# Kernel optimization log

Hardware: AMD Instinct MI355X
Metric: run time of the kernel (lower is better)

## Reference

```python
import jax, jax.numpy as jnp
import numpy as np

NEG_SLOPE = 0.2  # PyG GATv2Conv default leaky_relu negative slope


def _gatv2_layer(x, src, dst, n, Wl, bl, Wr, br, att, bias, concat):
    # PyG GATv2Conv (share_weights=False, edge_dim=None):
    #   x_l = lin_l(x) on source, x_r = lin_r(x) on target
    #   m = leaky_relu(x_l[src] + x_r[dst]); alpha = softmax_dst(<m, att>)
    #   out[i] = sum_{e: dst=i} alpha_e * x_l[src_e]
    H, C = att.shape
    xl = (x @ Wl + bl).reshape(n, H, C)
    xr = (x @ Wr + br).reshape(n, H, C)
    m = jax.nn.leaky_relu(xl[src] + xr[dst], NEG_SLOPE)      # [E,H,C]
    logits = jnp.einsum('ehc,hc->eh', m, att)                # [E,H]
    lmax = jax.ops.segment_max(logits, dst, num_segments=n)  # [N,H]
    e = jnp.exp(logits - lmax[dst])
    denom = jax.ops.segment_sum(e, dst, num_segments=n)
    alpha = e / (denom[dst] + 1e-16)                         # [E,H]
    out = jax.ops.segment_sum(xl[src] * alpha[:, :, None], dst, num_segments=n)
    out = out.reshape(n, H * C) if concat else out.mean(axis=1)
    return out + bias


def _glorot(key, shape):
    fan_in, fan_out = shape[0], shape[-1]
    s = jnp.sqrt(6.0 / (fan_in + fan_out))
    return jax.random.uniform(key, shape, jnp.float32, -s, s)


def setup_inputs() -> dict:
    key = jax.random.key(0)
    N, E, B = 50000, 800000, 512
    node_in, hidden, heads, meta_dim = 128, 32, 4, 12
    ks = jax.random.split(key, 32)
    inp = {
        'x': jax.random.normal(ks[0], (N, node_in), jnp.float32),
        'edge_index': jax.random.randint(ks[1], (2, E), 0, N, jnp.int64),
        'batch': jnp.sort(jax.random.randint(ks[2], (N,), 0, B, jnp.int64)),
        'metadata': jax.random.normal(ks[3], (B, meta_dim), jnp.float32),
    }
    dims = [(node_in, hidden, heads), (hidden * heads, hidden, heads), (hidden * heads, hidden, 1)]
    i = 4
    for li, (din, dh, H) in enumerate(dims):
        inp[f'Wl{li}'] = _glorot(ks[i], (din, H * dh)); i += 1
        inp[f'bl{li}'] = jnp.zeros((H * dh,), jnp.float32)
        inp[f'Wr{li}'] = _glorot(ks[i], (din, H * dh)); i += 1
        inp[f'br{li}'] = jnp.zeros((H * dh,), jnp.float32)
        inp[f'att{li}'] = _glorot(ks[i], (H, dh)); i += 1
        out_dim = H * dh if li < 2 else dh  # last layer concat=False
        inp[f'b{li}'] = jnp.zeros((out_dim,), jnp.float32)
    pool_dim = hidden  # n_layers=3 -> final single-head layer
    inp['Wh1'] = _glorot(ks[i], (pool_dim + meta_dim, pool_dim)); i += 1
    inp['bh1'] = jnp.zeros((pool_dim,), jnp.float32)
    inp['Wh2'] = _glorot(ks[i], (pool_dim, 1)); i += 1
    inp['bh2'] = jnp.zeros((1,), jnp.float32)
    return inp


def reference(x, edge_index, batch, metadata,
              Wl0, bl0, Wr0, br0, att0, b0,
              Wl1, bl1, Wr1, br1, att1, b1,
              Wl2, bl2, Wr2, br2, att2, b2,
              Wh1, bh1, Wh2, bh2):
    n = x.shape[0]
    B = metadata.shape[0]
    # PyG GATv2Conv add_self_loops=True
    loop = jnp.arange(n, dtype=edge_index.dtype)
    src = jnp.concatenate([edge_index[0], loop])
    dst = jnp.concatenate([edge_index[1], loop])
    params = [(Wl0, bl0, Wr0, br0, att0, b0, True),
              (Wl1, bl1, Wr1, br1, att1, b1, True),
              (Wl2, bl2, Wr2, br2, att2, b2, False)]
    h = x
    for (Wl, bl, Wr, br, att, bias, concat) in params:
        h = _gatv2_layer(h, src, dst, n, Wl, bl, Wr, br, att, bias, concat)
        h = jax.nn.elu(h)  # dropout is identity in eval mode
    # global mean pool over graphs
    sums = jax.ops.segment_sum(h, batch, num_segments=B)
    cnt = jax.ops.segment_sum(jnp.ones((n,), h.dtype), batch, num_segments=B)
    emb = sums / jnp.clip(cnt, 1.0)[:, None]
    z = jnp.concatenate([emb, metadata], axis=1)
    z = jax.nn.relu(z @ Wh1 + bh1)
    return z @ Wh2 + bh2  # (B, 1) logits
```

## Files before the change

kernel.cpp:

```cpp
#include <hip/hip_runtime.h>
#include <cstdint>
#include <cstddef>

#define NEG_SLOPE 0.2f
#define LOG2E 1.44269504f
#define NBLK 256

typedef __attribute__((ext_vector_type(8))) short short8;
typedef __attribute__((ext_vector_type(4))) float f32x4;

__device__ __forceinline__ float bf2f(unsigned short u) {
    union { unsigned int i; float f; } x; x.i = ((unsigned int)u) << 16; return x.f;
}
__device__ __forceinline__ unsigned short f2bf(float f) {
    union { float f; unsigned int i; } x;
    x.f = f;
    unsigned int u = x.i;
    return (unsigned short)((u + 0x7FFFu + ((u >> 16) & 1u)) >> 16);
}

__device__ __forceinline__ float dpp_sum8(float p) {
    p += __int_as_float(__builtin_amdgcn_update_dpp(0, __float_as_int(p), 0xB1, 0xF, 0xF, true));
    p += __int_as_float(__builtin_amdgcn_update_dpp(0, __float_as_int(p), 0x4E, 0xF, 0xF, true));
    p += __int_as_float(__builtin_amdgcn_update_dpp(0, __float_as_int(p), 0x141, 0xF, 0xF, true));
    return p;
}

__global__ __launch_bounds__(256) void prep_w_all(
    const float* __restrict__ Wl0, const float* __restrict__ Wr0,
    const float* __restrict__ Wl1, const float* __restrict__ Wr1,
    const float* __restrict__ Wl2, const float* __restrict__ Wr2,
    unsigned short* __restrict__ Bt0, unsigned short* __restrict__ Bt1,
    unsigned short* __restrict__ Bt2)
{
    int idx = blockIdx.x * 256 + threadIdx.x;
    const int SZ = 256 * 128;
    const float *Wl, *Wr; unsigned short* Bt; int dout;
    if (idx < SZ)              { Wl = Wl0; Wr = Wr0; Bt = Bt0; dout = 128; }
    else if (idx < 2 * SZ)     { Wl = Wl1; Wr = Wr1; Bt = Bt1; dout = 128; idx -= SZ; }
    else if (idx < 2 * SZ + 64 * 128) { Wl = Wl2; Wr = Wr2; Bt = Bt2; dout = 32; idx -= 2 * SZ; }
    else return;
    int n = idx >> 7, k = idx & 127;
    float v = (n < dout) ? Wl[(size_t)k * dout + n] : Wr[(size_t)k * dout + (n - dout)];
    Bt[idx] = f2bf(v);
}

template<int BN, bool ABF16>
__global__ __launch_bounds__(256) void gemm_mfma(
    const void* __restrict__ Avoid, int M,
    const unsigned short* __restrict__ Bt,
    const float* __restrict__ bl, const float* __restrict__ br,
    int dout, unsigned short* __restrict__ XL, unsigned short* __restrict__ XR)
{
    constexpr int LDA = 136;
    constexpr int NT  = BN / 16;
    __shared__ __attribute__((aligned(16))) unsigned short Bs[BN * LDA];
    const int t  = threadIdx.x;
    const int m0 = blockIdx.x * 64;
    const int n0 = blockIdx.y * BN;

    const int w    = t >> 6;
    const int lane = t & 63;
    const int fr   = lane & 15;
    const int quad = lane >> 4;

#pragma unroll
    for (int i = 0; i < BN / 16; ++i) {
        int c  = t + i * 256;
        int n  = c >> 4;
        int kc = (c & 15) * 8;
        *(short8*)(Bs + n * LDA + kc) =
            *(const short8*)(Bt + (size_t)(n0 + n) * 128 + kc);
    }

    const int arow = m0 + w * 16 + fr;
    const size_t abase = (size_t)(arow < M ? arow : 0) * 128 + quad * 8;
    short8 afr[4];
    if (ABF16) {
        const unsigned short* A = (const unsigned short*)Avoid;
#pragma unroll
        for (int kk = 0; kk < 4; ++kk)
            afr[kk] = *(const short8*)(A + abase + kk * 32);
    } else {
        const float* A = (const float*)Avoid;
#pragma unroll
        for (int kk = 0; kk < 4; ++kk) {
            float4 lo = *(const float4*)(A + abase + kk * 32);
            float4 hi = *(const float4*)(A + abase + kk * 32 + 4);
            afr[kk][0] = (short)f2bf(lo.x); afr[kk][1] = (short)f2bf(lo.y);
            afr[kk][2] = (short)f2bf(lo.z); afr[kk][3] = (short)f2bf(lo.w);
            afr[kk][4] = (short)f2bf(hi.x); afr[kk][5] = (short)f2bf(hi.y);
            afr[kk][6] = (short)f2bf(hi.z); afr[kk][7] = (short)f2bf(hi.w);
        }
    }
    __syncthreads();

    f32x4 acc[NT] = {};
    const unsigned short* bp = Bs + fr * LDA + quad * 8;
#pragma unroll
    for (int kk = 0; kk < 4; ++kk) {
#pragma unroll
        for (int j = 0; j < NT; ++j) {
            short8 bfr = *(const short8*)(bp + j * 16 * LDA + kk * 32);
            acc[j] = __builtin_amdgcn_mfma_f32_16x16x32_bf16(afr[kk], bfr, acc[j], 0, 0, 0);
        }
    }

#pragma unroll
    for (int j = 0; j < NT; ++j) {
        int col = n0 + j * 16 + fr;
        float bias = (col < dout) ? bl[col] : br[col - dout];
#pragma unroll
        for (int r = 0; r < 4; ++r) {
            int row = m0 + w * 16 + quad * 4 + r;
            if (row < M) {
                unsigned short o = f2bf(acc[j][r] + bias);
                if (col < dout) XL[(size_t)row * dout + col] = o;
                else            XR[(size_t)row * dout + (col - dout)] = o;
            }
        }
    }
}

__global__ __launch_bounds__(256) void csr_hist(
    const int* __restrict__ dst, int E, int tile, int* __restrict__ hist)
{
    __shared__ int h[256];
    const int t = threadIdx.x, b = blockIdx.x;
    h[t] = 0;
    __syncthreads();
    const int e0 = b * tile;
    const int e1 = min(E, e0 + tile);
    for (int e = e0 + t; e < e1; e += 256)
        atomicAdd(&h[dst[e] >> 8], 1);
    __syncthreads();
    hist[t * NBLK + b] = h[t];
}

__global__ __launch_bounds__(256) void csr_scatter(
    const int* __restrict__ src, const int* __restrict__ dst, int E, int tile,
    const int* __restrict__ hist_s, unsigned int* __restrict__ sorted)
{
    __shared__ int cur[256];
    const int t = threadIdx.x, b = blockIdx.x;
    cur[t] = hist_s[t * NBLK + b];
    __syncthreads();
    const int e0 = b * tile;
    const int e1 = min(E, e0 + tile);
    for (int e = e0 + t; e < e1; e += 256) {
        int d = dst[e];
        int pos = atomicAdd(&cur[d >> 8], 1);
        sorted[pos] = ((unsigned int)d << 16) | (unsigned int)src[e];
    }
}

__global__ __launch_bounds__(256) void csr_fine(
    const unsigned int* __restrict__ sorted, int E, int N,
    const int* __restrict__ hist_s,
    int* __restrict__ rowptr, unsigned short* __restrict__ csr_src)
{
    __shared__ int h[256];
    __shared__ int sc[256];
    const int t = threadIdx.x, d = blockIdx.x;
    const int start = hist_s[d * NBLK];
    const int end   = (d < 255) ? hist_s[(d + 1) * NBLK] : E;
    h[t] = 0;
    __syncthreads();
    for (int e = start + t; e < end; e += 256)
        atomicAdd(&h[(sorted[e] >> 16) & 0xFF], 1);
    __syncthreads();
    int v = h[t];
    sc[t] = v;
    __syncthreads();
    for (int off = 1; off < 256; off <<= 1) {
        int u = (t >= off) ? sc[t - off] : 0;
        __syncthreads();
        sc[t] += u;
        __syncthreads();
    }
    const int base = start + sc[t] - v;
    const int node = (d << 8) + t;
    if (node <= N) rowptr[node] = base;
    h[t] = base;
    __syncthreads();
    for (int e = start + t; e < end; e += 256) {
        unsigned int it = sorted[e];
        int pos = atomicAdd(&h[(it >> 16) & 0xFF], 1);
        csr_src[pos] = (unsigned short)(it & 0xFFFFu);
    }
}

__global__ __launch_bounds__(256) void scan_partial(
    const int* __restrict__ cnt, int N, int* __restrict__ bsum)
{
    __shared__ int red[4];
    const int t = threadIdx.x;
    const int base = blockIdx.x * 2048;
    int s = 0;
#pragma unroll
    for (int i = 0; i < 8; ++i) {
        int idx = base + t + i * 256;
        if (idx < N) s += cnt[idx];
    }
#pragma unroll
    for (int off = 32; off >= 1; off >>= 1) s += __shfl_xor(s, off);
    if ((t & 63) == 0) red[t >> 6] = s;
    __syncthreads();
    if (t == 0) bsum[blockIdx.x] = red[0] + red[1] + red[2] + red[3];
}

__global__ __launch_bounds__(256) void scan_bsums(
    int* __restrict__ bsum, int nb, int E, int* __restrict__ rowptr, int N)
{
    __shared__ int sh[256];
    const int t = threadIdx.x;
    int v = (t < nb) ? bsum[t] : 0;
    sh[t] = v;
    __syncthreads();
    for (int off = 1; off < 256; off <<= 1) {
        int u = (t >= off) ? sh[t - off] : 0;
        __syncthreads();
        sh[t] += u;
        __syncthreads();
    }
    if (t < nb) bsum[t] = sh[t] - v;
    if (t == 0) rowptr[N] = E;
}

__global__ __launch_bounds__(256) void scan_final(
    const int* __restrict__ cnt, int N, const int* __restrict__ bsum,
    int* __restrict__ rowptr)
{
    __shared__ int sdat[2048];
    __shared__ int tsum[256];
    const int t = threadIdx.x;
    const int base = blockIdx.x * 2048;
#pragma unroll
    for (int i = 0; i < 8; ++i) {
        int idx = base + t + i * 256;
        sdat[t + i * 256] = (idx < N) ? cnt[idx] : 0;
    }
    __syncthreads();
    int vals[8];
    int s = 0;
#pragma unroll
    for (int j = 0; j < 8; ++j) { vals[j] = sdat[t * 8 + j]; s += vals[j]; }
    tsum[t] = s;
    __syncthreads();
    for (int off = 1; off < 256; off <<= 1) {
        int u = (t >= off) ? tsum[t - off] : 0;
        __syncthreads();
        tsum[t] += u;
        __syncthreads();
    }
    int run = bsum[blockIdx.x] + tsum[t] - s;
#pragma unroll
    for (int j = 0; j < 8; ++j) { sdat[t * 8 + j] = run; run += vals[j]; }
    __syncthreads();
#pragma unroll
    for (int i = 0; i < 8; ++i) {
        int idx = base + t + i * 256;
        if (idx < N) rowptr[idx] = sdat[t + i * 256];
    }
}

template<int H>
__global__ __launch_bounds__(256, 4) void gat_fused(
    const unsigned short* __restrict__ xl, const unsigned short* __restrict__ xr,
    const int* __restrict__ rowptr, const unsigned short* __restrict__ csr_src,
    const float* __restrict__ att, const float* __restrict__ bias,
    unsigned short* __restrict__ hout, int hstride, int N)
{
    constexpr int HC  = 32 * H;
    constexpr int LPE = HC / 4;
    constexpr int EPW = 64 / LPE;
    const int node = blockIdx.x * 4 + (threadIdx.x >> 6);
    if (node >= N) return;
    const int lane = threadIdx.x & 63;
    const int q    = lane % LPE;
    const int slot = lane / LPE;
    const int rs   = rowptr[node];
    const int re   = rowptr[node + 1];

    const unsigned short* __restrict__ xlb = xl + 4 * q;
    float4 xri;
    {
        ushort4 u = *(const ushort4*)(xr + (size_t)node * HC + 4 * q);
        xri.x = bf2f(u.x); xri.y = bf2f(u.y); xri.z = bf2f(u.z); xri.w = bf2f(u.w);
    }
    float4 b1, b2;
    {
        float4 a = *(const float4*)(att + 4 * q);
        const float c1 = 0.5f * (1.0f + NEG_SLOPE) * LOG2E;
        const float c2 = 0.5f * (1.0f - NEG_SLOPE) * LOG2E;
        b1.x = a.x * c1; b1.y = a.y * c1; b1.z = a.z * c1; b1.w = a.w * c1;
        b2.x = a.x * c2; b2.y = a.y * c2; b2.z = a.z * c2; b2.w = a.w * c2;
    }

    float l = 0.f;
    float4 acc = make_float4(0.f, 0.f, 0.f, 0.f);

    auto ld4 = [&](int s) -> float4 {
        ushort4 u = *(const ushort4*)(xlb + (size_t)s * HC);
        float4 v;
        v.x = bf2f(u.x); v.y = bf2f(u.y); v.z = bf2f(u.z); v.w = bf2f(u.w);
        return v;
    };

    auto edge_w = [&](const float4& v) -> float {
        float sx = v.x + xri.x, sy = v.y + xri.y, sz = v.z + xri.z, sw = v.w + xri.w;
        float p  = b1.x * sx;
        float pq = b2.x * fabsf(sx);
        p  = fmaf(b1.y, sy, p);
        pq = fmaf(b2.y, fabsf(sy), pq);
        p  = fmaf(b1.z, sz, p);
        pq = fmaf(b2.z, fabsf(sz), pq);
        p  = fmaf(b1.w, sw, p);
        pq = fmaf(b2.w, fabsf(sw), pq);
        p += pq;
        p = dpp_sum8(p);
        return exp2f(p);
    };

    if (slot == 0) {
        float4 v = ld4(node);
        float w = edge_w(v);
        l = w;
        acc.x = w * v.x; acc.y = w * v.y; acc.z = w * v.z; acc.w = w * v.w;
    }

    int k = rs + slot;
    for (; k + EPW < re; k += 2 * EPW) {
        int s0 = csr_src[k];
        int s1 = csr_src[k + EPW];
        float4 v0 = ld4(s0);
        float4 v1 = ld4(s1);
        float w0 = edge_w(v0);
        float w1 = edge_w(v1);
        l += w0 + w1;
        acc.x = fmaf(w0, v0.x, fmaf(w1, v1.x, acc.x));
        acc.y = fmaf(w0, v0.y, fmaf(w1, v1.y, acc.y));
        acc.z = fmaf(w0, v0.z, fmaf(w1, v1.z, acc.z));
        acc.w = fmaf(w0, v0.w, fmaf(w1, v1.w, acc.w));
    }
    if (k < re) {
        int s0 = csr_src[k];
        float4 v0 = ld4(s0);
        float w0 = edge_w(v0);
        l += w0;
        acc.x = fmaf(w0, v0.x, acc.x);
        acc.y = fmaf(w0, v0.y, acc.y);
        acc.z = fmaf(w0, v0.z, acc.z);
        acc.w = fmaf(w0, v0.w, acc.w);
    }

#pragma unroll
    for (int mask = LPE; mask < 64; mask <<= 1) {
        l     += __shfl_xor(l, mask);
        acc.x += __shfl_xor(acc.x, mask);
        acc.y += __shfl_xor(acc.y, mask);
        acc.z += __shfl_xor(acc.z, mask);
        acc.w += __shfl_xor(acc.w, mask);
    }

    if (lane < LPE) {
        const float4 bi = *(const float4*)(bias + 4 * q);
        float inv = 1.f / (l + 1e-16f);
        float4 o;
        o.x = acc.x * inv + bi.x;
        o.y = acc.y * inv + bi.y;
        o.z = acc.z * inv + bi.z;
        o.w = acc.w * inv + bi.w;
        o.x = (o.x > 0.f) ? o.x : expm1f(o.x);
        o.y = (o.y > 0.f) ? o.y : expm1f(o.y);
        o.z = (o.z > 0.f) ? o.z : expm1f(o.z);
        o.w = (o.w > 0.f) ? o.w : expm1f(o.w);
        ushort4 ob;
        ob.x = f2bf(o.x); ob.y = f2bf(o.y); ob.z = f2bf(o.z); ob.w = f2bf(o.w);
        *(ushort4*)(hout + (size_t)node * hstride + 4 * q) = ob;
    }
}

__global__ __launch_bounds__(128) void pool_head_kernel(
    const unsigned short* __restrict__ h, int hstride,
    const int* __restrict__ batch, int N,
    const float* __restrict__ meta,
    const float* __restrict__ Wh1, const float* __restrict__ bh1,
    const float* __restrict__ Wh2, const float* __restrict__ bh2,
    float* __restrict__ out)
{
    const int b = blockIdx.x;
    const int t = threadIdx.x;
    __shared__ float s[128];
    __shared__ float z[44];

    int lo = 0, hi = N;
    while (lo < hi) { int mid = (lo + hi) >> 1; if (batch[mid] < b) lo = mid + 1; else hi = mid; }
    int lo2 = lo, hi2 = N;
    while (lo2 < hi2) { int mid = (lo2 + hi2) >> 1; if (batch[mid] < b + 1) lo2 = mid + 1; else hi2 = mid; }
    const int start = lo, end = lo2;

    const int c = t & 31, r = t >> 5;
    float acc = 0.f;
    for (int row = start + r; row < end; row += 4)
        acc += bf2f(h[(size_t)row * hstride + c]);
    s[t] = acc;
    __syncthreads();
    if (t < 32) {
        float sum = s[t] + s[t + 32] + s[t + 64] + s[t + 96];
        z[t] = sum / fmaxf((float)(end - start), 1.0f);
    } else if (t < 44) {
        z[t] = meta[(size_t)b * 12 + (t - 32)];
    }
    __syncthreads();
    if (t < 32) {
        float hj = bh1[t];
#pragma unroll
        for (int k = 0; k < 44; ++k)
            hj = fmaf(z[k], Wh1[k * 32 + t], hj);
        hj = fmaxf(hj, 0.f);
        float p = hj * Wh2[t];
#pragma unroll
        for (int off = 16; off >= 1; off >>= 1)
            p += __shfl_xor(p, off, 32);
        if (t == 0) out[b] = p + bh2[0];
    }
}

extern "C" void kernel_launch(void* const* d_in, const int* in_sizes, int n_in,
                              void* d_out, int out_size, void* d_ws, size_t ws_size,
                              hipStream_t stream)
{
    const float* x     = (const float*)d_in[0];
    const int*   ei    = (const int*)d_in[1];
    const int*   batch = (const int*)d_in[2];
    const float* meta  = (const float*)d_in[3];
    const float* Wl[3]  = {(const float*)d_in[4],  (const float*)d_in[10], (const float*)d_in[16]};
    const float* bl[3]  = {(const float*)d_in[5],  (const float*)d_in[11], (const float*)d_in[17]};
    const float* Wr[3]  = {(const float*)d_in[6],  (const float*)d_in[12], (const float*)d_in[18]};
    const float* br[3]  = {(const float*)d_in[7],  (const float*)d_in[13], (const float*)d_in[19]};
    const float* att[3] = {(const float*)d_in[8],  (const float*)d_in[14], (const float*)d_in[20]};
    const float* bb[3]  = {(const float*)d_in[9],  (const float*)d_in[15], (const float*)d_in[21]};
    const float* Wh1 = (const float*)d_in[22];
    const float* bh1 = (const float*)d_in[23];
    const float* Wh2 = (const float*)d_in[24];
    const float* bh2 = (const float*)d_in[25];
    float* out = (float*)d_out;

    const int N  = in_sizes[0] / 128;
    const int E  = in_sizes[1] / 2;
    const int B  = in_sizes[3] / 12;

    char* wsp = (char*)d_ws;
    size_t off_ = 0;
    auto alloc = [&](size_t bytes) {
        char* p = wsp + off_;
        off_ = (off_ + bytes + 255) & ~(size_t)255;
        return p;
    };
    unsigned short* xlbuf = (unsigned short*)alloc((size_t)N * 128 * 2);
    unsigned short* xrbuf = (unsigned short*)alloc((size_t)N * 128 * 2);
    unsigned short* hbuf  = (unsigned short*)alloc((size_t)N * 128 * 2);
    int*   rowptr  = (int*)alloc((size_t)(N + 1) * 4);
    unsigned short* csr_src = (unsigned short*)alloc((size_t)E * 2);
    unsigned int*   sorted  = (unsigned int*)alloc((size_t)E * 4);
    int*   hist_g  = (int*)alloc((size_t)65536 * 4);
    int*   hist_s  = (int*)alloc((size_t)65537 * 4);
    unsigned short* Bt0     = (unsigned short*)alloc((size_t)256 * 128 * 2);
    unsigned short* Bt1     = (unsigned short*)alloc((size_t)256 * 128 * 2);
    unsigned short* Bt2     = (unsigned short*)alloc((size_t)64 * 128 * 2);
    int*   bsum    = (int*)alloc((size_t)256 * 4);

    const int* srcI = ei;
    const int* dstI = ei + E;

    prep_w_all<<<(2 * 256 * 128 + 64 * 128 + 255) / 256, 256, 0, stream>>>(
        Wl[0], Wr[0], Wl[1], Wr[1], Wl[2], Wr[2], Bt0, Bt1, Bt2);

    const int tile = (E + NBLK - 1) / NBLK;
    csr_hist<<<NBLK, 256, 0, stream>>>(dstI, E, tile, hist_g);
    scan_partial<<<32, 256, 0, stream>>>(hist_g, 65536, bsum);
    scan_bsums<<<1, 256, 0, stream>>>(bsum, 32, E, hist_s, 65536);
    scan_final<<<32, 256, 0, stream>>>(hist_g, 65536, bsum, hist_s);
    csr_scatter<<<NBLK, 256, 0, stream>>>(srcI, dstI, E, tile, hist_s, sorted);
    csr_fine<<<(N >> 8) + 1, 256, 0, stream>>>(sorted, E, N, hist_s, rowptr, csr_src);

    const int GB = (N + 3) / 4;
    const int MB = (N + 63) / 64;

    {
        gemm_mfma<128, false><<<dim3(MB, 2), 256, 0, stream>>>(x, N, Bt0, bl[0], br[0], 128, xlbuf, xrbuf);
        gat_fused<4><<<GB, 256, 0, stream>>>(xlbuf, xrbuf, rowptr, csr_src, att[0], bb[0], hbuf, 128, N);
    }
    {
        gemm_mfma<128, true><<<dim3(MB, 2), 256, 0, stream>>>(hbuf, N, Bt1, bl[1], br[1], 128, xlbuf, xrbuf);
        gat_fused<4><<<GB, 256, 0, stream>>>(xlbuf, xrbuf, rowptr, csr_src, att[1], bb[1], hbuf, 128, N);
    }
    {
        gemm_mfma<64, true><<<dim3(MB, 1), 256, 0, stream>>>(hbuf, N, Bt2, bl[2], br[2], 32, xlbuf, xrbuf);
        gat_fused<1><<<GB, 256, 0, stream>>>(xlbuf, xrbuf, rowptr, csr_src, att[2], bb[2], hbuf, 32, N);
    }
    pool_head_kernel<<<B, 128, 0, stream>>>(hbuf, 32, batch, N, meta, Wh1, bh1, Wh2, bh2, out);
}
```

Baseline: 340.8 us.

## Merge all stages into one cooperative persistent megakernel with grid syncs

Result: slower. 1.147 ms (+236.5%).

```diff
diff --git a/kernel.cpp b/kernel.cpp
--- a/kernel.cpp
+++ b/kernel.cpp
@@ -1,10 +1,13 @@
 #include <hip/hip_runtime.h>
+#include <hip/hip_cooperative_groups.h>
 #include <cstdint>
 #include <cstddef>
 
+namespace cg = cooperative_groups;
+
 #define NEG_SLOPE 0.2f
 #define LOG2E 1.44269504f
-#define NBLK 256
+#define SMEM_BYTES 17408
 
 typedef __attribute__((ext_vector_type(8))) short short8;
 typedef __attribute__((ext_vector_type(4))) float f32x4;
@@ -26,223 +29,56 @@
     return p;
 }
 
-__global__ __launch_bounds__(256) void prep_w_all(
-    const float* __restrict__ Wl0, const float* __restrict__ Wr0,
-    const float* __restrict__ Wl1, const float* __restrict__ Wr1,
-    const float* __restrict__ Wl2, const float* __restrict__ Wr2,
-    unsigned short* __restrict__ Bt0, unsigned short* __restrict__ Bt1,
-    unsigned short* __restrict__ Bt2)
-{
-    int idx = blockIdx.x * 256 + threadIdx.x;
+struct KParams {
+    const float* x; const int* srcI; const int* dstI; const int* batch; const float* meta;
+    const float *Wl0, *bl0, *Wr0, *br0, *att0, *b0;
+    const float *Wl1, *bl1, *Wr1, *br1, *att1, *b1;
+    const float *Wl2, *bl2, *Wr2, *br2, *att2, *b2;
+    const float *Wh1, *bh1, *Wh2, *bh2;
+    float* out;
+    unsigned short *xlbuf, *xrbuf, *hbuf, *csr_src, *Bt0, *Bt1, *Bt2;
+    int *rowptr, *hist_g, *hist_s, *bsum;
+    unsigned int* sorted;
+    int N, E, B, tile;
+};
+
+
+__device__ __forceinline__ void phase_prep_hist(const KParams& p, unsigned char* smem) {
+    const int t = threadIdx.x;
+    int* h = (int*)smem;
+    if (blockIdx.x < 256) {
+        h[t] = 0;
+        __syncthreads();
+        const int e0 = blockIdx.x * p.tile;
+        const int e1 = min(p.E, e0 + p.tile);
+        for (int e = e0 + t; e < e1; e += 256)
+            atomicAdd(&h[p.dstI[e] >> 8], 1);
+        __syncthreads();
+        p.hist_g[t * 256 + blockIdx.x] = h[t];
+    }
     const int SZ = 256 * 128;
-    const float *Wl, *Wr; unsigned short* Bt; int dout;
-    if (idx < SZ)              { Wl = Wl0; Wr = Wr0; Bt = Bt0; dout = 128; }
-    else if (idx < 2 * SZ)     { Wl = Wl1; Wr = Wr1; Bt = Bt1; dout = 128; idx -= SZ; }
-    else if (idx < 2 * SZ + 64 * 128) { Wl = Wl2; Wr = Wr2; Bt = Bt2; dout = 32; idx -= 2 * SZ; }
-    else return;
-    int n = idx >> 7, k = idx & 127;
-    float v = (n < dout) ? Wl[(size_t)k * dout + n] : Wr[(size_t)k * dout + (n - dout)];
-    Bt[idx] = f2bf(v);
-}
-
-template<int BN, bool ABF16>
-__global__ __launch_bounds__(256) void gemm_mfma(
-    const void* __restrict__ Avoid, int M,
-    const unsigned short* __restrict__ Bt,
-    const float* __restrict__ bl, const float* __restrict__ br,
-    int dout, unsigned short* __restrict__ XL, unsigned short* __restrict__ XR)
-{
-    constexpr int LDA = 136;
-    constexpr int NT  = BN / 16;
-    __shared__ __attribute__((aligned(16))) unsigned short Bs[BN * LDA];
-    const int t  = threadIdx.x;
-    const int m0 = blockIdx.x * 64;
-    const int n0 = blockIdx.y * BN;
-
-    const int w    = t >> 6;
-    const int lane = t & 63;
-    const int fr   = lane & 15;
-    const int quad = lane >> 4;
-
-#pragma unroll
-    for (int i = 0; i < BN / 16; ++i) {
-        int c  = t + i * 256;
-        int n  = c >> 4;
-        int kc = (c & 15) * 8;
-        *(short8*)(Bs + n * LDA + kc) =
-            *(const short8*)(Bt + (size_t)(n0 + n) * 128 + kc);
-    }
-
-    const int arow = m0 + w * 16 + fr;
-    const size_t abase = (size_t)(arow < M ? arow : 0) * 128 + quad * 8;
-    short8 afr[4];
-    if (ABF16) {
-        const unsigned short* A = (const unsigned short*)Avoid;
-#pragma unroll
-        for (int kk = 0; kk < 4; ++kk)
-            afr[kk] = *(const short8*)(A + abase + kk * 32);
-    } else {
-        const float* A = (const float*)Avoid;
-#pragma unroll
-        for (int kk = 0; kk < 4; ++kk) {
-            float4 lo = *(const float4*)(A + abase + kk * 32);
-            float4 hi = *(const float4*)(A + abase + kk * 32 + 4);
-            afr[kk][0] = (short)f2bf(lo.x); afr[kk][1] = (short)f2bf(lo.y);
-            afr[kk][2] = (short)f2bf(lo.z); afr[kk][3] = (short)f2bf(lo.w);
-            afr[kk][4] = (short)f2bf(hi.x); afr[kk][5] = (short)f2bf(hi.y);
-            afr[kk][6] = (short)f2bf(hi.z); afr[kk][7] = (short)f2bf(hi.w);
-        }
-    }
-    __syncthreads();
-
-    f32x4 acc[NT] = {};
-    const unsigned short* bp = Bs + fr * LDA + quad * 8;
-#pragma unroll
-    for (int kk = 0; kk < 4; ++kk) {
-#pragma unroll
-        for (int j = 0; j < NT; ++j) {
-            short8 bfr = *(const short8*)(bp + j * 16 * LDA + kk * 32);
-            acc[j] = __builtin_amdgcn_mfma_f32_16x16x32_bf16(afr[kk], bfr, acc[j], 0, 0, 0);
-        }
-    }
-
-#pragma unroll
-    for (int j = 0; j < NT; ++j) {
-        int col = n0 + j * 16 + fr;
-        float bias = (col < dout) ? bl[col] : br[col - dout];
-#pragma unroll
-        for (int r = 0; r < 4; ++r) {
-            int row = m0 + w * 16 + quad * 4 + r;
-            if (row < M) {
-                unsigned short o = f2bf(acc[j][r] + bias);
-                if (col < dout) XL[(size_t)row * dout + col] = o;
-                else            XR[(size_t)row * dout + (col - dout)] = o;
-            }
-        }
-    }
-}
-
-__global__ __launch_bounds__(256) void csr_hist(
-    const int* __restrict__ dst, int E, int tile, int* __restrict__ hist)
-{
-    __shared__ int h[256];
-    const int t = threadIdx.x, b = blockIdx.x;
-    h[t] = 0;
-    __syncthreads();
-    const int e0 = b * tile;
-    const int e1 = min(E, e0 + tile);
-    for (int e = e0 + t; e < e1; e += 256)
-        atomicAdd(&h[dst[e] >> 8], 1);
-    __syncthreads();
-    hist[t * NBLK + b] = h[t];
-}
-
-__global__ __launch_bounds__(256) void csr_scatter(
-    const int* __restrict__ src, const int* __restrict__ dst, int E, int tile,
-    const int* __restrict__ hist_s, unsigned int* __restrict__ sorted)
-{
-    __shared__ int cur[256];
-    const int t = threadIdx.x, b = blockIdx.x;
-    cur[t] = hist_s[t * NBLK + b];
-    __syncthreads();
-    const int e0 = b * tile;
-    const int e1 = min(E, e0 + tile);
-    for (int e = e0 + t; e < e1; e += 256) {
-        int d = dst[e];
-        int pos = atomicAdd(&cur[d >> 8], 1);
-        sorted[pos] = ((unsigned int)d << 16) | (unsigned int)src[e];
-    }
-}
-
-__global__ __launch_bounds__(256) void csr_fine(
-    const unsigned int* __restrict__ sorted, int E, int N,
-    const int* __restrict__ hist_s,
-    int* __restrict__ rowptr, unsigned short* __restrict__ csr_src)
-{
-    __shared__ int h[256];
-    __shared__ int sc[256];
-    const int t = threadIdx.x, d = blockIdx.x;
-    const int start = hist_s[d * NBLK];
-    const int end   = (d < 255) ? hist_s[(d + 1) * NBLK] : E;
-    h[t] = 0;
-    __syncthreads();
-    for (int e = start + t; e < end; e += 256)
-        atomicAdd(&h[(sorted[e] >> 16) & 0xFF], 1);
-    __syncthreads();
-    int v = h[t];
-    sc[t] = v;
-    __syncthreads();
-    for (int off = 1; off < 256; off <<= 1) {
-        int u = (t >= off) ? sc[t - off] : 0;
-        __syncthreads();
-        sc[t] += u;
-        __syncthreads();
-    }
-    const int base = start + sc[t] - v;
-    const int node = (d << 8) + t;
-    if (node <= N) rowptr[node] = base;
-    h[t] = base;
-    __syncthreads();
-    for (int e = start + t; e < end; e += 256) {
-        unsigned int it = sorted[e];
-        int pos = atomicAdd(&h[(it >> 16) & 0xFF], 1);
-        csr_src[pos] = (unsigned short)(it & 0xFFFFu);
-    }
-}
-
-__global__ __launch_bounds__(256) void scan_partial(
-    const int* __restrict__ cnt, int N, int* __restrict__ bsum)
-{
-    __shared__ int red[4];
+    for (int idx0 = blockIdx.x * 256 + t; idx0 < 2 * SZ + 64 * 128; idx0 += gridDim.x * 256) {
+        int idx = idx0;
+        const float *Wl, *Wr; unsigned short* Bt; int dout;
+        if (idx < SZ)          { Wl = p.Wl0; Wr = p.Wr0; Bt = p.Bt0; dout = 128; }
+        else if (idx < 2 * SZ) { Wl = p.Wl1; Wr = p.Wr1; Bt = p.Bt1; dout = 128; idx -= SZ; }
+        else                   { Wl = p.Wl2; Wr = p.Wr2; Bt = p.Bt2; dout = 32;  idx -= 2 * SZ; }
+        int n = idx >> 7, k = idx & 127;
+        float v = (n < dout) ? Wl[(size_t)k * dout + n] : Wr[(size_t)k * dout + (n - dout)];
+        Bt[idx] = f2bf(v);
+    }
+}
+
+__device__ __forceinline__ void phase_scanA(const KParams& p, unsigned char* smem) {
+    if (blockIdx.x >= 32) return;
+    int* sdat = (int*)smem;
+    int* tsum = (int*)(smem + 8192);
     const int t = threadIdx.x;
     const int base = blockIdx.x * 2048;
-    int s = 0;
-#pragma unroll
-    for (int i = 0; i < 8; ++i) {
-        int idx = base + t + i * 256;
-        if (idx < N) s += cnt[idx];
-    }
-#pragma unroll
-    for (int off = 32; off >= 1; off >>= 1) s += __shfl_xor(s, off);
-    if ((t & 63) == 0) red[t >> 6] = s;
+#pragma unroll
+    for (int i = 0; i < 8; ++i) sdat[t + i * 256] = p.hist_g[base + t + i * 256];
     __syncthreads();
-    if (t == 0) bsum[blockIdx.x] = red[0] + red[1] + red[2] + red[3];
-}
-
-__global__ __launch_bounds__(256) void scan_bsums(
-    int* __restrict__ bsum, int nb, int E, int* __restrict__ rowptr, int N)
-{
-    __shared__ int sh[256];
-    const int t = threadIdx.x;
-    int v = (t < nb) ? bsum[t] : 0;
-    sh[t] = v;
-    __syncthreads();
-    for (int off = 1; off < 256; off <<= 1) {
-        int u = (t >= off) ? sh[t - off] : 0;
-        __syncthreads();
-        sh[t] += u;
-        __syncthreads();
-    }
-    if (t < nb) bsum[t] = sh[t] - v;
-    if (t == 0) rowptr[N] = E;
-}
-
-__global__ __launch_bounds__(256) void scan_final(
-    const int* __restrict__ cnt, int N, const int* __restrict__ bsum,
-    int* __restrict__ rowptr)
-{
-    __shared__ int sdat[2048];
-    __shared__ int tsum[256];
-    const int t = threadIdx.x;
-    const int base = blockIdx.x * 2048;
-#pragma unroll
-    for (int i = 0; i < 8; ++i) {
-        int idx = base + t + i * 256;
-        sdat[t + i * 256] = (idx < N) ? cnt[idx] : 0;
-    }
-    __syncthreads();
-    int vals[8];
-    int s = 0;
+    int vals[8]; int s = 0;
 #pragma unroll
     for (int j = 0; j < 8; ++j) { vals[j] = sdat[t * 8 + j]; s += vals[j]; }
     tsum[t] = s;
@@ -253,19 +89,169 @@
         tsum[t] += u;
         __syncthreads();
     }
-    int run = bsum[blockIdx.x] + tsum[t] - s;
+    if (t == 0) p.bsum[blockIdx.x] = tsum[255];
+    int run = tsum[t] - s;
 #pragma unroll
     for (int j = 0; j < 8; ++j) { sdat[t * 8 + j] = run; run += vals[j]; }
     __syncthreads();
 #pragma unroll
-    for (int i = 0; i < 8; ++i) {
-        int idx = base + t + i * 256;
-        if (idx < N) rowptr[idx] = sdat[t + i * 256];
+    for (int i = 0; i < 8; ++i) p.hist_s[base + t + i * 256] = sdat[t + i * 256];
+}
+
+__device__ __forceinline__ void phase_scanB(const KParams& p) {
+    const int t = threadIdx.x;
+    if (blockIdx.x == 0 && t < 32) {
+        int o = p.bsum[t];
+        int v = o;
+#pragma unroll
+        for (int off = 1; off < 32; off <<= 1) {
+            int u = __shfl_up(v, off);
+            if (t >= off) v += u;
+        }
+        p.bsum[t] = v - o;
+    }
+}
+
+__device__ __forceinline__ void phase_scanC(const KParams& p) {
+    if (blockIdx.x >= 32) return;
+    const int t = threadIdx.x;
+    const int add = p.bsum[blockIdx.x];
+    const int base = blockIdx.x * 2048;
+#pragma unroll
+    for (int i = 0; i < 8; ++i) p.hist_s[base + t + i * 256] += add;
+}
+
+__device__ __forceinline__ void phase_scatter(const KParams& p, unsigned char* smem) {
+    if (blockIdx.x >= 256) return;
+    int* cur = (int*)smem;
+    const int t = threadIdx.x;
+    cur[t] = p.hist_s[t * 256 + blockIdx.x];
+    __syncthreads();
+    const int e0 = blockIdx.x * p.tile;
+    const int e1 = min(p.E, e0 + p.tile);
+    for (int e = e0 + t; e < e1; e += 256) {
+        int d = p.dstI[e];
+        int pos = atomicAdd(&cur[d >> 8], 1);
+        p.sorted[pos] = ((unsigned int)d << 16) | (unsigned int)p.srcI[e];
+    }
+}
+
+__device__ __forceinline__ void phase_fine(const KParams& p, unsigned char* smem) {
+    int* h  = (int*)smem;
+    int* sc = (int*)(smem + 1024);
+    const int t = threadIdx.x;
+    const int nb = (p.N >> 8) + 1;
+    for (int d = blockIdx.x; d < nb; d += gridDim.x) {
+        __syncthreads();
+        const int start = p.hist_s[d * 256];
+        const int end   = (d < 255) ? p.hist_s[(d + 1) * 256] : p.E;
+        h[t] = 0;
+        __syncthreads();
+        for (int e = start + t; e < end; e += 256)
+            atomicAdd(&h[(p.sorted[e] >> 16) & 0xFF], 1);
+        __syncthreads();
+        int v = h[t];
+        sc[t] = v;
+        __syncthreads();
+        for (int off = 1; off < 256; off <<= 1) {
+            int u = (t >= off) ? sc[t - off] : 0;
+            __syncthreads();
+            sc[t] += u;
+            __syncthreads();
+        }
+        const int base = start + sc[t] - v;
+        const int node = (d << 8) + t;
+        if (node <= p.N) p.rowptr[node] = base;
+        h[t] = base;
+        __syncthreads();
+        for (int e = start + t; e < end; e += 256) {
+            unsigned int it = p.sorted[e];
+            int pos = atomicAdd(&h[(it >> 16) & 0xFF], 1);
+            p.csr_src[pos] = (unsigned short)(it & 0xFFFFu);
+        }
+    }
+}
+
+__device__ __forceinline__ void gemm_phase(
+    const void* Avoid, int M, bool abf16,
+    const unsigned short* __restrict__ Bt,
+    const float* __restrict__ bl, const float* __restrict__ br,
+    int dout, int lognyt, unsigned short* __restrict__ XL, unsigned short* __restrict__ XR,
+    unsigned char* smem)
+{
+    unsigned short* Bs = (unsigned short*)smem;
+    const int t    = threadIdx.x;
+    const int w    = t >> 6;
+    const int lane = t & 63;
+    const int fr   = lane & 15;
+    const int quad = lane >> 4;
+    const int mb = (M + 63) >> 6;
+    const int ntiles = mb << lognyt;
+    const int nymask = (1 << lognyt) - 1;
+
+    for (int tid = blockIdx.x; tid < ntiles; tid += gridDim.x) {
+        const int m0 = (tid >> lognyt) * 64;
+        const int n0 = (tid & nymask) * 64;
+        __syncthreads();
+#pragma unroll
+        for (int i = 0; i < 4; ++i) {
+            int c  = t + i * 256;
+            int n  = c >> 4;
+            int kc = (c & 15) * 8;
+            *(short8*)(Bs + n * 136 + kc) =
+                *(const short8*)(Bt + (size_t)(n0 + n) * 128 + kc);
+        }
+        const int arow = m0 + w * 16 + fr;
+        const size_t abase = (size_t)(arow < M ? arow : 0) * 128 + quad * 8;
+        short8 afr[4];
+        if (abf16) {
+            const unsigned short* A = (const unsigned short*)Avoid;
+#pragma unroll
+            for (int kk = 0; kk < 4; ++kk)
+                afr[kk] = *(const short8*)(A + abase + kk * 32);
+        } else {
+            const float* A = (const float*)Avoid;
+#pragma unroll
+            for (int kk = 0; kk < 4; ++kk) {
+                float4 lo = *(const float4*)(A + abase + kk * 32);
+                float4 hi = *(const float4*)(A + abase + kk * 32 + 4);
+                afr[kk][0] = (short)f2bf(lo.x); afr[kk][1] = (short)f2bf(lo.y);
+                afr[kk][2] = (short)f2bf(lo.z); afr[kk][3] = (short)f2bf(lo.w);
+                afr[kk][4] = (short)f2bf(hi.x); afr[kk][5] = (short)f2bf(hi.y);
+                afr[kk][6] = (short)f2bf(hi.z); afr[kk][7] = (short)f2bf(hi.w);
+            }
+        }
+        __syncthreads();
+
+        f32x4 acc[4] = {};
+        const unsigned short* bp = Bs + fr * 136 + quad * 8;
+#pragma unroll
+        for (int kk = 0; kk < 4; ++kk) {
+#pragma unroll
+            for (int j = 0; j < 4; ++j) {
+                short8 bfr = *(const short8*)(bp + j * 16 * 136 + kk * 32);
+                acc[j] = __builtin_amdgcn_mfma_f32_16x16x32_bf16(afr[kk], bfr, acc[j], 0, 0, 0);
+            }
+        }
+#pragma unroll
+        for (int j = 0; j < 4; ++j) {
+            int col = n0 + j * 16 + fr;
+            float bias = (col < dout) ? bl[col] : br[col - dout];
+#pragma unroll
+            for (int r = 0; r < 4; ++r) {
+                int row = m0 + w * 16 + quad * 4 + r;
+                if (row < M) {
+                    unsigned short o = f2bf(acc[j][r] + bias);
+                    if (col < dout) XL[(size_t)row * dout + col] = o;
+                    else            XR[(size_t)row * dout + (col - dout)] = o;
+                }
+            }
+        }
     }
 }
 
 template<int H>
-__global__ __launch_bounds__(256, 4) void gat_fused(
+__device__ __forceinline__ void gat_phase(
     const unsigned short* __restrict__ xl, const unsigned short* __restrict__ xr,
     const int* __restrict__ rowptr, const unsigned short* __restrict__ csr_src,
     const float* __restrict__ att, const float* __restrict__ bias,
@@ -274,179 +260,218 @@
     constexpr int HC  = 32 * H;
     constexpr int LPE = HC / 4;
     constexpr int EPW = 64 / LPE;
-    const int node = blockIdx.x * 4 + (threadIdx.x >> 6);
-    if (node >= N) return;
-    const int lane = threadIdx.x & 63;
-    const int q    = lane % LPE;
-    const int slot = lane / LPE;
-    const int rs   = rowptr[node];
-    const int re   = rowptr[node + 1];
-
-    const unsigned short* __restrict__ xlb = xl + 4 * q;
-    float4 xri;
-    {
-        ushort4 u = *(const ushort4*)(xr + (size_t)node * HC + 4 * q);
-        xri.x = bf2f(u.x); xri.y = bf2f(u.y); xri.z = bf2f(u.z); xri.w = bf2f(u.w);
-    }
-    float4 b1, b2;
-    {
-        float4 a = *(const float4*)(att + 4 * q);
-        const float c1 = 0.5f * (1.0f + NEG_SLOPE) * LOG2E;
-        const float c2 = 0.5f * (1.0f - NEG_SLOPE) * LOG2E;
-        b1.x = a.x * c1; b1.y = a.y * c1; b1.z = a.z * c1; b1.w = a.w * c1;
-        b2.x = a.x * c2; b2.y = a.y * c2; b2.z = a.z * c2; b2.w = a.w * c2;
-    }
-
-    float l = 0.f;
-    float4 acc = make_float4(0.f, 0.f, 0.f, 0.f);
-
-    auto ld4 = [&](int s) -> float4 {
-        ushort4 u = *(const ushort4*)(xlb + (size_t)s * HC);
-        float4 v;
-        v.x = bf2f(u.x); v.y = bf2f(u.y); v.z = bf2f(u.z); v.w = bf2f(u.w);
-        return v;
-    };
-
-    auto edge_w = [&](const float4& v) -> float {
-        float sx = v.x + xri.x, sy = v.y + xri.y, sz = v.z + xri.z, sw = v.w + xri.w;
-        float p  = b1.x * sx;
-        float pq = b2.x * fabsf(sx);
-        p  = fmaf(b1.y, sy, p);
-        pq = fmaf(b2.y, fabsf(sy), pq);
-        p  = fmaf(b1.z, sz, p);
-        pq = fmaf(b2.z, fabsf(sz), pq);
-        p  = fmaf(b1.w, sw, p);
-        pq = fmaf(b2.w, fabsf(sw), pq);
-        p += pq;
-        p = dpp_sum8(p);
-        return exp2f(p);
-    };
-
-    if (slot == 0) {
-        float4 v = ld4(node);
-        float w = edge_w(v);
-        l = w;
-        acc.x = w * v.x; acc.y = w * v.y; acc.z = w * v.z; acc.w = w * v.w;
-    }
-
-    int k = rs + slot;
-    for (; k + EPW < re; k += 2 * EPW) {
-        int s0 = csr_src[k];
-        int s1 = csr_src[k + EPW];
-        float4 v0 = ld4(s0);
-        float4 v1 = ld4(s1);
-        float w0 = edge_w(v0);
-        float w1 = edge_w(v1);
-        l += w0 + w1;
-        acc.x = fmaf(w0, v0.x, fmaf(w1, v1.x, acc.x));
-        acc.y = fmaf(w0, v0.y, fmaf(w1, v1.y, acc.y));
-        acc.z = fmaf(w0, v0.z, fmaf(w1, v1.z, acc.z));
-        acc.w = fmaf(w0, v0.w, fmaf(w1, v1.w, acc.w));
-    }
-    if (k < re) {
-        int s0 = csr_src[k];
-        float4 v0 = ld4(s0);
-        float w0 = edge_w(v0);
-        l += w0;
-        acc.x = fmaf(w0, v0.x, acc.x);
-        acc.y = fmaf(w0, v0.y, acc.y);
-        acc.z = fmaf(w0, v0.z, acc.z);
-        acc.w = fmaf(w0, v0.w, acc.w);
-    }
-
-#pragma unroll
-    for (int mask = LPE; mask < 64; mask <<= 1) {
-        l     += __shfl_xor(l, mask);
-        acc.x += __shfl_xor(acc.x, mask);
-        acc.y += __shfl_xor(acc.y, mask);
-        acc.z += __shfl_xor(acc.z, mask);
-        acc.w += __shfl_xor(acc.w, mask);
-    }
-
-    if (lane < LPE) {
-        const float4 bi = *(const float4*)(bias + 4 * q);
-        float inv = 1.f / (l + 1e-16f);
-        float4 o;
-        o.x = acc.x * inv + bi.x;
-        o.y = acc.y * inv + bi.y;
-        o.z = acc.z * inv + bi.z;
-        o.w = acc.w * inv + bi.w;
-        o.x = (o.x > 0.f) ? o.x : expm1f(o.x);
-        o.y = (o.y > 0.f) ? o.y : expm1f(o.y);
-        o.z = (o.z > 0.f) ? o.z : expm1f(o.z);
-        o.w = (o.w > 0.f) ? o.w : expm1f(o.w);
-        ushort4 ob;
-        ob.x = f2bf(o.x); ob.y = f2bf(o.y); ob.z = f2bf(o.z); ob.w = f2bf(o.w);
-        *(ushort4*)(hout + (size_t)node * hstride + 4 * q) = ob;
-    }
-}
-
-__global__ __launch_bounds__(128) void pool_head_kernel(
-    const unsigned short* __restrict__ h, int hstride,
-    const int* __restrict__ batch, int N,
-    const float* __restrict__ meta,
-    const float* __restrict__ Wh1, const float* __restrict__ bh1,
-    const float* __restrict__ Wh2, const float* __restrict__ bh2,
-    float* __restrict__ out)
-{
-    const int b = blockIdx.x;
-    const int t = threadIdx.x;
-    __shared__ float s[128];
-    __shared__ float z[44];
-
-    int lo = 0, hi = N;
-    while (lo < hi) { int mid = (lo + hi) >> 1; if (batch[mid] < b) lo = mid + 1; else hi = mid; }
-    int lo2 = lo, hi2 = N;
-    while (lo2 < hi2) { int mid = (lo2 + hi2) >> 1; if (batch[mid] < b + 1) lo2 = mid + 1; else hi2 = mid; }
-    const int start = lo, end = lo2;
-
-    const int c = t & 31, r = t >> 5;
-    float acc = 0.f;
-    for (int row = start + r; row < end; row += 4)
-        acc += bf2f(h[(size_t)row * hstride + c]);
-    s[t] = acc;
-    __syncthreads();
-    if (t < 32) {
-        float sum = s[t] + s[t + 32] + s[t + 64] + s[t + 96];
-        z[t] = sum / fmaxf((float)(end - start), 1.0f);
-    } else if (t < 44) {
-        z[t] = meta[(size_t)b * 12 + (t - 32)];
-    }
-    __syncthreads();
-    if (t < 32) {
-        float hj = bh1[t];
-#pragma unroll
-        for (int k = 0; k < 44; ++k)
-            hj = fmaf(z[k], Wh1[k * 32 + t], hj);
-        hj = fmaxf(hj, 0.f);
-        float p = hj * Wh2[t];
-#pragma unroll
-        for (int off = 16; off >= 1; off >>= 1)
-            p += __shfl_xor(p, off, 32);
-        if (t == 0) out[b] = p + bh2[0];
-    }
+    const int ngrp = (N + 3) >> 2;
+    for (int grp = blockIdx.x; grp < ngrp; grp += gridDim.x) {
+        const int node = grp * 4 + (threadIdx.x >> 6);
+        if (node >= N) continue;
+        const int lane = threadIdx.x & 63;
+        const int q    = lane % LPE;
+        const int slot = lane / LPE;
+        const int rs   = rowptr[node];
+        const int re   = rowptr[node + 1];
+
+        const unsigned short* __restrict__ xlb = xl + 4 * q;
+        float4 xri;
+        {
+            ushort4 u = *(const ushort4*)(xr + (size_t)node * HC + 4 * q);
+            xri.x = bf2f(u.x); xri.y = bf2f(u.y); xri.z = bf2f(u.z); xri.w = bf2f(u.w);
+        }
+        float4 b1, b2;
+        {
+            float4 a = *(const float4*)(att + 4 * q);
+            const float c1 = 0.5f * (1.0f + NEG_SLOPE) * LOG2E;
+            const float c2 = 0.5f * (1.0f - NEG_SLOPE) * LOG2E;
+            b1.x = a.x * c1; b1.y = a.y * c1; b1.z = a.z * c1; b1.w = a.w * c1;
+            b2.x = a.x * c2; b2.y = a.y * c2; b2.z = a.z * c2; b2.w = a.w * c2;
+        }
+
+        float l = 0.f;
+        float4 acc = make_float4(0.f, 0.f, 0.f, 0.f);
+
+        auto ld4 = [&](int s) -> float4 {
+            ushort4 u = *(const ushort4*)(xlb + (size_t)s * HC);
+            float4 v;
+            v.x = bf2f(u.x); v.y = bf2f(u.y); v.z = bf2f(u.z); v.w = bf2f(u.w);
+            return v;
+        };
+        auto edge_w = [&](const float4& v) -> float {
+            float sx = v.x + xri.x, sy = v.y + xri.y, sz = v.z + xri.z, sw = v.w + xri.w;
+            float p  = b1.x * sx;
+            float pq = b2.x * fabsf(sx);
+            p  = fmaf(b1.y, sy, p);
+            pq = fmaf(b2.y, fabsf(sy), pq);
+            p  = fmaf(b1.z, sz, p);
+            pq = fmaf(b2.z, fabsf(sz), pq);
+            p  = fmaf(b1.w, sw, p);
+            pq = fmaf(b2.w, fabsf(sw), pq);
+            p += pq;
+            p = dpp_sum8(p);
+            return exp2f(p);
+        };
+
+        if (slot == 0) {
+            float4 v = ld4(node);
+            float w = edge_w(v);
+            l = w;
+            acc.x = w * v.x; acc.y = w * v.y; acc.z = w * v.z; acc.w = w * v.w;
+        }
+        int k = rs + slot;
+        for (; k + EPW < re; k += 2 * EPW) {
+            int s0 = csr_src[k];
+            int s1 = csr_src[k + EPW];
+            float4 v0 = ld4(s0);
+            float4 v1 = ld4(s1);
+            float w0 = edge_w(v0);
+            float w1 = edge_w(v1);
+            l += w0 + w1;
+            acc.x = fmaf(w0, v0.x, fmaf(w1, v1.x, acc.x));
+            acc.y = fmaf(w0, v0.y, fmaf(w1, v1.y, acc.y));
+            acc.z = fmaf(w0, v0.z, fmaf(w1, v1.z, acc.z));
+            acc.w = fmaf(w0, v0.w, fmaf(w1, v1.w, acc.w));
+        }
+        if (k < re) {
+            int s0 = csr_src[k];
+            float4 v0 = ld4(s0);
+            float w0 = edge_w(v0);
+            l += w0;
+            acc.x = fmaf(w0, v0.x, acc.x);
+            acc.y = fmaf(w0, v0.y, acc.y);
+            acc.z = fmaf(w0, v0.z, acc.z);
+            acc.w = fmaf(w0, v0.w, acc.w);
+        }
+#pragma unroll
+        for (int mask = LPE; mask < 64; mask <<= 1) {
+            l     += __shfl_xor(l, mask);
+            acc.x += __shfl_xor(acc.x, mask);
+            acc.y += __shfl_xor(acc.y, mask);
+            acc.z += __shfl_xor(acc.z, mask);
+            acc.w += __shfl_xor(acc.w, mask);
+        }
+        if (lane < LPE) {
+            const float4 bi = *(const float4*)(bias + 4 * q);
+            float inv = 1.f / (l + 1e-16f);
+            float4 o;
+            o.x = acc.x * inv + bi.x;
+            o.y = acc.y * inv + bi.y;
+            o.z = acc.z * inv + bi.z;
+            o.w = acc.w * inv + bi.w;
+            o.x = (o.x > 0.f) ? o.x : expm1f(o.x);
+            o.y = (o.y > 0.f) ? o.y : expm1f(o.y);
+            o.z = (o.z > 0.f) ? o.z : expm1f(o.z);
+            o.w = (o.w > 0.f) ? o.w : expm1f(o.w);
+            ushort4 ob;
+            ob.x = f2bf(o.x); ob.y = f2bf(o.y); ob.z = f2bf(o.z); ob.w = f2bf(o.w);
+            *(ushort4*)(hout + (size_t)node * hstride + 4 * q) = ob;
+        }
+    }
+}
+
+__device__ __forceinline__ void pool_phase(const KParams& p, unsigned char* smem) {
+    float* s = (float*)smem;
+    float* z = (float*)(smem + 1024);
+    const int t    = threadIdx.x;
+    const int half = t >> 7;
+    const int tl   = t & 127;
+    for (int g0 = blockIdx.x * 2; g0 < p.B; g0 += gridDim.x * 2) {
+        __syncthreads();
+        const int b = g0 + half;
+        const bool active = b < p.B;
+        int start = 0, end = 0;
+        if (active) {
+            int lo = 0, hi = p.N;
+            while (lo < hi) { int mid = (lo + hi) >> 1; if (p.batch[mid] < b) lo = mid + 1; else hi = mid; }
+            int lo2 = lo, hi2 = p.N;
+            while (lo2 < hi2) { int mid = (lo2 + hi2) >> 1; if (p.batch[mid] < b + 1) lo2 = mid + 1; else hi2 = mid; }
+            start = lo; end = lo2;
+        }
+        const int c = tl & 31, r = tl >> 5;
+        float acc = 0.f;
+        for (int row = start + r; row < end; row += 4)
+            acc += bf2f(p.hbuf[(size_t)row * 32 + c]);
+        s[t] = acc;
+        __syncthreads();
+        if (tl < 32) {
+            float sum = s[half * 128 + tl] + s[half * 128 + tl + 32]
+                      + s[half * 128 + tl + 64] + s[half * 128 + tl + 96];
+            z[half * 44 + tl] = sum / fmaxf((float)(end - start), 1.0f);
+        } else if (tl < 44 && active) {
+            z[half * 44 + tl] = p.meta[(size_t)b * 12 + (tl - 32)];
+        }
+        __syncthreads();
+        if (tl < 32 && active) {
+            float hj = p.bh1[tl];
+#pragma unroll
+            for (int k = 0; k < 44; ++k)
+                hj = fmaf(z[half * 44 + k], p.Wh1[k * 32 + tl], hj);
+            hj = fmaxf(hj, 0.f);
+            float pr = hj * p.Wh2[tl];
+#pragma unroll
+            for (int off = 16; off >= 1; off >>= 1)
+                pr += __shfl_xor(pr, off, 32);
+            if (tl == 0) p.out[b] = pr + p.bh2[0];
+        }
+    }
+}
+
+__global__ __launch_bounds__(256) void mega(KParams p) {
+    cg::grid_group gg = cg::this_grid();
+    __shared__ __attribute__((aligned(16))) unsigned char smem[SMEM_BYTES];
+
+    phase_prep_hist(p, smem);                                   gg.sync();
+    phase_scanA(p, smem);                                       gg.sync();
+    phase_scanB(p);                                             gg.sync();
+    phase_scanC(p);                                             gg.sync();
+    phase_scatter(p, smem);                                     gg.sync();
+    phase_fine(p, smem);                                        gg.sync();
+    gemm_phase(p.x,    p.N, false, p.Bt0, p.bl0, p.br0, 128, 2, p.xlbuf, p.xrbuf, smem); gg.sync();
+    gat_phase<4>(p.xlbuf, p.xrbuf, p.rowptr, p.csr_src, p.att0, p.b0, p.hbuf, 128, p.N); gg.sync();
+    gemm_phase(p.hbuf, p.N, true,  p.Bt1, p.bl1, p.br1, 128, 2, p.xlbuf, p.xrbuf, smem); gg.sync();
+    gat_phase<4>(p.xlbuf, p.xrbuf, p.rowptr, p.csr_src, p.att1, p.b1, p.hbuf, 128, p.N); gg.sync();
+    gemm_phase(p.hbuf, p.N, true,  p.Bt2, p.bl2, p.br2, 32,  0, p.xlbuf, p.xrbuf, smem); gg.sync();
+    gat_phase<1>(p.xlbuf, p.xrbuf, p.rowptr, p.csr_src, p.att2, p.b2, p.hbuf, 32,  p.N); gg.sync();
+    pool_phase(p, smem);
+}
+
+__global__ __launch_bounds__(256) void fb_p0(KParams p) {
+    __shared__ __attribute__((aligned(16))) unsigned char smem[SMEM_BYTES];
+    phase_prep_hist(p, smem);
+}
+__global__ __launch_bounds__(256) void fb_scanA(KParams p) {
+    __shared__ __attribute__((aligned(16))) unsigned char smem[SMEM_BYTES];
+    phase_scanA(p, smem);
+}
+__global__ __launch_bounds__(256) void fb_scanB(KParams p) { phase_scanB(p); }
+__global__ __launch_bounds__(256) void fb_scanC(KParams p) { phase_scanC(p); }
+__global__ __launch_bounds__(256) void fb_scatter(KParams p) {
+    __shared__ __attribute__((aligned(16))) unsigned char smem[SMEM_BYTES];
+    phase_scatter(p, smem);
+}
+__global__ __launch_bounds__(256) void fb_fine(KParams p) {
+    __shared__ __attribute__((aligned(16))) unsigned char smem[SMEM_BYTES];
+    phase_fine(p, smem);
+}
+__global__ __launch_bounds__(256) void fb_gemm(KParams p, int layer) {
+    __shared__ __attribute__((aligned(16))) unsigned char smem[SMEM_BYTES];
+    if (layer == 0)      gemm_phase(p.x,    p.N, false, p.Bt0, p.bl0, p.br0, 128, 2, p.xlbuf, p.xrbuf, smem);
+    else if (layer == 1) gemm_phase(p.hbuf, p.N, true,  p.Bt1, p.bl1, p.br1, 128, 2, p.xlbuf, p.xrbuf, smem);
+    else                 gemm_phase(p.hbuf, p.N, true,  p.Bt2, p.bl2, p.br2, 32,  0, p.xlbuf, p.xrbuf, smem);
+}
+__global__ __launch_bounds__(256) void fb_gat4(KParams p, int layer) {
+    if (layer == 0) gat_phase<4>(p.xlbuf, p.xrbuf, p.rowptr, p.csr_src, p.att0, p.b0, p.hbuf, 128, p.N);
+    else            gat_phase<4>(p.xlbuf, p.xrbuf, p.rowptr, p.csr_src, p.att1, p.b1, p.hbuf, 128, p.N);
+}
+__global__ __launch_bounds__(256) void fb_gat1(KParams p) {
+    gat_phase<1>(p.xlbuf, p.xrbuf, p.rowptr, p.csr_src, p.att2, p.b2, p.hbuf, 32, p.N);
+}
+__global__ __launch_bounds__(256) void fb_pool(KParams p) {
+    __shared__ __attribute__((aligned(16))) unsigned char smem[SMEM_BYTES];
+    pool_phase(p, smem);
 }
 
 extern "C" void kernel_launch(void* const* d_in, const int* in_sizes, int n_in,
                               void* d_out, int out_size, void* d_ws, size_t ws_size,
                               hipStream_t stream)
 {
-    const float* x     = (const float*)d_in[0];
-    const int*   ei    = (const int*)d_in[1];
-    const int*   batch = (const int*)d_in[2];
-    const float* meta  = (const float*)d_in[3];
-    const float* Wl[3]  = {(const float*)d_in[4],  (const float*)d_in[10], (const float*)d_in[16]};
-    const float* bl[3]  = {(const float*)d_in[5],  (const float*)d_in[11], (const float*)d_in[17]};
-    const float* Wr[3]  = {(const float*)d_in[6],  (const float*)d_in[12], (const float*)d_in[18]};
-    const float* br[3]  = {(const float*)d_in[7],  (const float*)d_in[13], (const float*)d_in[19]};
-    const float* att[3] = {(const float*)d_in[8],  (const float*)d_in[14], (const float*)d_in[20]};
-    const float* bb[3]  = {(const float*)d_in[9],  (const float*)d_in[15], (const float*)d_in[21]};
-    const float* Wh1 = (const float*)d_in[22];
-    const float* bh1 = (const float*)d_in[23];
-    const float* Wh2 = (const float*)d_in[24];
-    const float* bh2 = (const float*)d_in[25];
-    float* out = (float*)d_out;
-
     const int N  = in_sizes[0] / 128;
     const int E  = in_sizes[1] / 2;
     const int B  = in_sizes[3] / 12;
@@ -454,51 +479,72 @@
     char* wsp = (char*)d_ws;
     size_t off_ = 0;
     auto alloc = [&](size_t bytes) {
-        char* p = wsp + off_;
+        char* ptr = wsp + off_;
         off_ = (off_ + bytes + 255) & ~(size_t)255;
-        return p;
+        return ptr;
     };
-    unsigned short* xlbuf = (unsigned short*)alloc((size_t)N * 128 * 2);
-    unsigned short* xrbuf = (unsigned short*)alloc((size_t)N * 128 * 2);
-    unsigned short* hbuf  = (unsigned short*)alloc((size_t)N * 128 * 2);
-    int*   rowptr  = (int*)alloc((size_t)(N + 1) * 4);
-    unsigned short* csr_src = (unsigned short*)alloc((size_t)E * 2);
-    unsigned int*   sorted  = (unsigned int*)alloc((size_t)E * 4);
-    int*   hist_g  = (int*)alloc((size_t)65536 * 4);
-    int*   hist_s  = (int*)alloc((size_t)65537 * 4);
-    unsigned short* Bt0     = (unsigned short*)alloc((size_t)256 * 128 * 2);
-    unsigned short* Bt1     = (unsigned short*)alloc((size_t)256 * 128 * 2);
-    unsigned short* Bt2     = (unsigned short*)alloc((size_t)64 * 128 * 2);
-    int*   bsum    = (int*)alloc((size_t)256 * 4);
-
-    const int* srcI = ei;
-    const int* dstI = ei + E;
-
-    prep_w_all<<<(2 * 256 * 128 + 64 * 128 + 255) / 256, 256, 0, stream>>>(
-        Wl[0], Wr[0], Wl[1], Wr[1], Wl[2], Wr[2], Bt0, Bt1, Bt2);
-
-    const int tile = (E + NBLK - 1) / NBLK;
-    csr_hist<<<NBLK, 256, 0, stream>>>(dstI, E, tile, hist_g);
-    scan_partial<<<32, 256, 0, stream>>>(hist_g, 65536, bsum);
-    scan_bsums<<<1, 256, 0, stream>>>(bsum, 32, E, hist_s, 65536);
-    scan_final<<<32, 256, 0, stream>>>(hist_g, 65536, bsum, hist_s);
-    csr_scatter<<<NBLK, 256, 0, stream>>>(srcI, dstI, E, tile, hist_s, sorted);
-    csr_fine<<<(N >> 8) + 1, 256, 0, stream>>>(sorted, E, N, hist_s, rowptr, csr_src);
-
-    const int GB = (N + 3) / 4;
-    const int MB = (N + 63) / 64;
-
-    {
-        gemm_mfma<128, false><<<dim3(MB, 2), 256, 0, stream>>>(x, N, Bt0, bl[0], br[0], 128, xlbuf, xrbuf);
-        gat_fused<4><<<GB, 256, 0, stream>>>(xlbuf, xrbuf, rowptr, csr_src, att[0], bb[0], hbuf, 128, N);
-    }
-    {
-        gemm_mfma<128, true><<<dim3(MB, 2), 256, 0, stream>>>(hbuf, N, Bt1, bl[1], br[1], 128, xlbuf, xrbuf);
-        gat_fused<4><<<GB, 256, 0, stream>>>(xlbuf, xrbuf, rowptr, csr_src, att[1], bb[1], hbuf, 128, N);
-    }
-    {
-        gemm_mfma<64, true><<<dim3(MB, 1), 256, 0, stream>>>(hbuf, N, Bt2, bl[2], br[2], 32, xlbuf, xrbuf);
-        gat_fused<1><<<GB, 256, 0, stream>>>(xlbuf, xrbuf, rowptr, csr_src, att[2], bb[2], hbuf, 32, N);
-    }
-    pool_head_kernel<<<B, 128, 0, stream>>>(hbuf, 32, batch, N, meta, Wh1, bh1, Wh2, bh2, out);
-}
+
+    KParams p;
+    p.x     = (const float*)d_in[0];
+    p.srcI  = (const int*)d_in[1];
+    p.dstI  = (const int*)d_in[1] + E;
+    p.batch = (const int*)d_in[2];
+    p.meta  = (const float*)d_in[3];
+    p.Wl0 = (const float*)d_in[4];  p.bl0 = (const float*)d_in[5];
+    p.Wr0 = (const float*)d_in[6];  p.br0 = (const float*)d_in[7];
+    p.att0 = (const float*)d_in[8]; p.b0  = (const float*)d_in[9];
+    p.Wl1 = (const float*)d_in[10]; p.bl1 = (const float*)d_in[11];
+    p.Wr1 = (const float*)d_in[12]; p.br1 = (const float*)d_in[13];
+    p.att1 = (const float*)d_in[14]; p.b1 = (const float*)d_in[15];
+    p.Wl2 = (const float*)d_in[16]; p.bl2 = (const float*)d_in[17];
+    p.Wr2 = (const float*)d_in[18]; p.br2 = (const float*)d_in[19];
+    p.att2 = (const float*)d_in[20]; p.b2 = (const float*)d_in[21];
+    p.Wh1 = (const float*)d_in[22]; p.bh1 = (const float*)d_in[23];
+    p.Wh2 = (const float*)d_in[24]; p.bh2 = (const float*)d_in[25];
+    p.out = (float*)d_out;
+
+    p.xlbuf  = (unsigned short*)alloc((size_t)N * 128 * 2);
+    p.xrbuf  = (unsigned short*)alloc((size_t)N * 128 * 2);
+    p.hbuf   = (unsigned short*)alloc((size_t)N * 128 * 2);
+    p.rowptr = (int*)alloc((size_t)(N + 1) * 4);
+    p.csr_src = (unsigned short*)alloc((size_t)E * 2);
+    p.sorted  = (unsigned int*)alloc((size_t)E * 4);
+    p.hist_g  = (int*)alloc((size_t)65536 * 4);
+    p.hist_s  = (int*)alloc((size_t)65537 * 4);
+    p.bsum    = (int*)alloc((size_t)256 * 4);
+    p.Bt0     = (unsigned short*)alloc((size_t)256 * 128 * 2);
+    p.Bt1     = (unsigned short*)alloc((size_t)256 * 128 * 2);
+    p.Bt2     = (unsigned short*)alloc((size_t)64 * 128 * 2);
+    p.N = N; p.E = E; p.B = B;
+    p.tile = (E + 255) / 256;
+
+    int occ = 0;
+    hipError_t qe = hipOccupancyMaxActiveBlocksPerMultiprocessor(
+        &occ, reinterpret_cast<const void*>(&mega), 256, 0);
+    if (qe != hipSuccess || occ < 1) occ = 2;
+    int G = 256 * occ;
+    if (G > 2048) G = 2048;
+    if (G < 256)  G = 256;
+
+    void* args[] = { (void*)&p };
+    hipError_t le = hipLaunchCooperativeKernel(
+        reinterpret_cast<void*>(&mega), dim3(G), dim3(256), args, 0, stream);
+
+    if (le != hipSuccess) {
+        const int ngemm = ((N + 63) / 64) * 4;
+        const int ngat  = (N + 3) / 4;
+        fb_p0<<<288, 256, 0, stream>>>(p);
+        fb_scanA<<<32, 256, 0, stream>>>(p);
+        fb_scanB<<<1, 256, 0, stream>>>(p);
+        fb_scanC<<<32, 256, 0, stream>>>(p);
+        fb_scatter<<<256, 256, 0, stream>>>(p);
+        fb_fine<<<(N >> 8) + 1, 256, 0, stream>>>(p);
+        fb_gemm<<<ngemm, 256, 0, stream>>>(p, 0);
+        fb_gat4<<<ngat, 256, 0, stream>>>(p, 0);
+        fb_gemm<<<ngemm, 256, 0, stream>>>(p, 1);
+        fb_gat4<<<ngat, 256, 0, stream>>>(p, 1);
+        fb_gemm<<<ngemm, 256, 0, stream>>>(p, 2);
+        fb_gat1<<<ngat, 256, 0, stream>>>(p);
+        fb_pool<<<(B + 1) / 2, 256, 0, stream>>>(p);
+    }
+}
```
